# Kernel optimization log

Hardware: AMD Instinct MI355X
Metric: run time of the kernel (lower is better)

## Reference

```python
import jax, jax.numpy as jnp
import numpy as np

N_NODES = 256
BATCH = 1024
N_LAYERS = 2  # total linear layers = N_LAYERS + 1, each followed by tanh


def setup_inputs() -> dict:
    key = jax.random.key(0)
    ks = jax.random.split(key, 4)
    scale = 1.0 / np.sqrt(N_NODES)
    x = jax.random.normal(ks[0], (BATCH, N_NODES), dtype=jnp.float32)
    # nn.Linear weights: [out_features, in_features], no bias
    W0 = jax.random.normal(ks[1], (N_NODES, N_NODES), dtype=jnp.float32) * scale
    W1 = jax.random.normal(ks[2], (N_NODES, N_NODES), dtype=jnp.float32) * scale
    W2 = jax.random.normal(ks[3], (N_NODES, N_NODES), dtype=jnp.float32) * scale
    return {"x": x, "W0": W0, "W1": W1, "W2": W2}


def reference(x, W0, W1, W2):
    # Original loop: for each node i, zero out column i of x (x @ Par with
    # Par = I - e_i e_i^T), run the 3-layer tanh MLP, keep output column i.
    # Vectorized: build all N masked copies at once.
    N = x.shape[1]
    mask = (1.0 - jnp.eye(N, dtype=x.dtype))  # [i, j]: zero col j==i
    Xm = x[None, :, :] * mask[:, None, :]     # [N, B, N]
    # nn.Linear: y = h @ W.T ; tanh after every layer (incl. last)
    h = jnp.tanh(jnp.einsum('ibn,mn->ibm', Xm, W0))
    h = jnp.tanh(jnp.einsum('ibn,mn->ibm', h, W1))
    h = jnp.tanh(jnp.einsum('ibn,mn->ibm', h, W2))  # [N, B, N]
    # f_x[b, i] = h[i, b, i]
    f_x = jnp.einsum('ibi->bi', h)
    return f_x
```

## Files before the change

### kernel.cpp

```cpp
#include <hip/hip_runtime.h>
#include <hip/hip_bf16.h>

#define N_NODES 256
#define BATCH   1024

typedef __attribute__((ext_vector_type(8))) short bf16x8;
typedef __attribute__((ext_vector_type(4))) float f32x4;

__device__ __forceinline__ float ftanh(float x) {
    float e = __builtin_amdgcn_exp2f(x * 2.8853900817779268f);
    float r = __builtin_amdgcn_rcpf(e + 1.0f);
    return fmaf(-2.0f, r, 1.0f);
}

__device__ __forceinline__ unsigned short f2bf(float f) {
    unsigned u = __float_as_uint(f);
    return (unsigned short)((u + 0x7fffu + ((u >> 16) & 1u)) >> 16);
}

__device__ __forceinline__ unsigned pack_bf2(float a, float b) {
    union { __hip_bfloat162 h; unsigned u; } cvt;
    cvt.h = __float22bfloat162_rn(make_float2(a, b));
    return cvt.u;
}

template <int CTRL>
__device__ __forceinline__ float dpp_add(float s) {
    int t = __builtin_amdgcn_update_dpp(0, __float_as_int(s), CTRL, 0xf, 0xf, true);
    return s + __int_as_float(t);
}

__global__ void z0_prep(const float* __restrict__ x, const float* __restrict__ W0,
                        const float* __restrict__ W1, float* __restrict__ Z0,
                        float* __restrict__ xT, float* __restrict__ W0col,
                        unsigned short* __restrict__ W1bf) {
    __shared__ float xs[32][36];
    __shared__ float ws[32][36];
    int t = threadIdx.x;

    int gb = (blockIdx.y * 32 + blockIdx.x) * 256 + t;
    {
        int i = gb >> 8, m = gb & 255;
        W0col[gb] = W0[m * 256 + i];
        W1bf[gb]  = f2bf(W1[gb]);
    }
#pragma unroll
    for (int r = 0; r < 4; ++r) {
        int id = r * 65536 + gb;
        int i = id >> 10, b = id & 1023;
        xT[id] = x[b * 256 + i];
    }

    int b0 = blockIdx.x * 32, m0 = blockIdx.y * 32;
    int lr = t >> 3, lc = (t & 7) << 2;
    int tr = (t >> 4) << 1, tc = (t & 15) << 1;
    float acc00 = 0.f, acc01 = 0.f, acc10 = 0.f, acc11 = 0.f;
    for (int k0 = 0; k0 < 256; k0 += 32) {
        *(float4*)&xs[lr][lc] = *(const float4*)&x[(b0 + lr) * 256 + k0 + lc];
        *(float4*)&ws[lr][lc] = *(const float4*)&W0[(m0 + lr) * 256 + k0 + lc];
        __syncthreads();
#pragma unroll
        for (int k = 0; k < 32; ++k) {
            float a0 = xs[tr][k], a1 = xs[tr + 1][k];
            float w0v = ws[tc][k], w1v = ws[tc + 1][k];
            acc00 = fmaf(a0, w0v, acc00);
            acc01 = fmaf(a0, w1v, acc01);
            acc10 = fmaf(a1, w0v, acc10);
            acc11 = fmaf(a1, w1v, acc11);
        }
        __syncthreads();
    }
    Z0[(b0 + tr) * 256 + m0 + tc]         = acc00;
    Z0[(b0 + tr) * 256 + m0 + tc + 1]     = acc01;
    Z0[(b0 + tr + 1) * 256 + m0 + tc]     = acc10;
    Z0[(b0 + tr + 1) * 256 + m0 + tc + 1] = acc11;
}

__launch_bounds__(512, 4)
__global__ void fused(const float* __restrict__ Z0, const float* __restrict__ xT,
                      const float* __restrict__ W0col,
                      const unsigned short* __restrict__ W1bf,
                      const float* __restrict__ W2, float* __restrict__ out) {
    __shared__ __align__(16) unsigned char h0s[64 * 512];
    float* wavepart = (float*)h0s;
    int t  = threadIdx.x;
    int r0 = blockIdx.x * 64;
    int i  = blockIdx.y;

    int wave = t >> 6, lane = t & 63;
    int lr = lane & 15, lh = lane >> 4;

    float w2v[2];
#pragma unroll
    for (int nt = 0; nt < 2; ++nt)
        w2v[nt] = W2[i * 256 + wave * 32 + nt * 16 + lr];

    {
        int rowgrp = t >> 5, chunk = t & 31;
        int col0 = chunk << 3;
        float4 w0a = *(const float4*)&W0col[i * 256 + col0];
        float4 w0b = *(const float4*)&W0col[i * 256 + col0 + 4];
        float w[8] = {w0a.x, w0a.y, w0a.z, w0a.w, w0b.x, w0b.y, w0b.z, w0b.w};
#pragma unroll
        for (int p = 0; p < 4; ++p) {
            int row = p * 16 + rowgrp;
            float xi = xT[i * 1024 + r0 + row];
            float4 za = *(const float4*)&Z0[(r0 + row) * 256 + col0];
            float4 zb = *(const float4*)&Z0[(r0 + row) * 256 + col0 + 4];
            float z[8] = {za.x, za.y, za.z, za.w, zb.x, zb.y, zb.z, zb.w};
            unsigned pk[4];
#pragma unroll
            for (int e = 0; e < 4; ++e) {
                float ha = ftanh(fmaf(-xi, w[2 * e],     z[2 * e]));
                float hb = ftanh(fmaf(-xi, w[2 * e + 1], z[2 * e + 1]));
                pk[e] = pack_bf2(ha, hb);
            }
            uint4 v = make_uint4(pk[0], pk[1], pk[2], pk[3]);
            *(uint4*)(h0s + row * 512 + (((chunk ^ (row & 31)) << 4))) = v;
        }
    }
    __syncthreads();

    f32x4 acc[4][2];
#pragma unroll
    for (int a = 0; a < 4; ++a)
#pragma unroll
        for (int b = 0; b < 2; ++b)
            acc[a][b] = (f32x4){0.f, 0.f, 0.f, 0.f};

    const unsigned short* w1p0 = W1bf + (wave * 32 + lr) * 256 + lh * 8;
    const unsigned short* w1p1 = W1bf + (wave * 32 + 16 + lr) * 256 + lh * 8;
    bf16x8 bnext0 = *(const bf16x8*)(w1p0);
    bf16x8 bnext1 = *(const bf16x8*)(w1p1);

#pragma unroll
    for (int ks = 0; ks < 8; ++ks) {
        int kk = ks * 32 + lh * 8;
        int chunk = kk >> 3;
        bf16x8 b0 = bnext0, b1 = bnext1;
        if (ks < 7) {
            bnext0 = *(const bf16x8*)(w1p0 + (ks + 1) * 32);
            bnext1 = *(const bf16x8*)(w1p1 + (ks + 1) * 32);
        }
        bf16x8 afrag[4];
#pragma unroll
        for (int mt = 0; mt < 4; ++mt) {
            int row = mt * 16 + lr;
            afrag[mt] = *(const bf16x8*)(h0s + row * 512 + ((chunk ^ (row & 31)) << 4));
        }
#pragma unroll
        for (int mt = 0; mt < 4; ++mt) {
            acc[mt][0] = __builtin_amdgcn_mfma_f32_16x16x32_bf16(
                afrag[mt], b0, acc[mt][0], 0, 0, 0);
            acc[mt][1] = __builtin_amdgcn_mfma_f32_16x16x32_bf16(
                afrag[mt], b1, acc[mt][1], 0, 0, 0);
        }
    }

    float part[4][4];
#pragma unroll
    for (int mt = 0; mt < 4; ++mt) {
#pragma unroll
        for (int r = 0; r < 4; ++r) {
            float s = fmaf(ftanh(acc[mt][0][r]), w2v[0],
                           ftanh(acc[mt][1][r]) * w2v[1]);
            s = dpp_add<0x118>(s);
            s = dpp_add<0x114>(s);
            s = dpp_add<0x112>(s);
            s = dpp_add<0x111>(s);
            part[mt][r] = s;
        }
    }
    __syncthreads();
    if (lr == 15) {
#pragma unroll
        for (int mt = 0; mt < 4; ++mt)
#pragma unroll
            for (int r = 0; r < 4; ++r)
                wavepart[wave * 64 + mt * 16 + lh * 4 + r] = part[mt][r];
    }
    __syncthreads();

    if (t < 64) {
        float s = 0.f;
#pragma unroll
        for (int w = 0; w < 8; ++w)
            s += wavepart[w * 64 + t];
        out[(r0 + t) * 256 + i] = ftanh(s);
    }
}

extern "C" void kernel_launch(void* const* d_in, const int* in_sizes, int n_in,
                              void* d_out, int out_size, void* d_ws, size_t ws_size,
                              hipStream_t stream) {
    const float* x  = (const float*)d_in[0];
    const float* W0 = (const float*)d_in[1];
    const float* W1 = (const float*)d_in[2];
    const float* W2 = (const float*)d_in[3];
    float* out = (float*)d_out;

    char* ws = (char*)d_ws;
    float* Z0            = (float*)ws;
    float* xT            = (float*)(ws + (1 << 20));
    float* W0col         = (float*)(ws + (2 << 20));
    unsigned short* W1bf = (unsigned short*)(ws + (2 << 20) + (256 << 10));

    z0_prep<<<dim3(32, 8), 256, 0, stream>>>(x, W0, W1, Z0, xT, W0col, W1bf);
    fused<<<dim3(16, 256), 512, 0, stream>>>(Z0, xT, W0col, W1bf, W2, out);
}
```

Before: 94.68 us.

## Process four nodes per block and overlap next h0 build with MFMA

Each block of the fused kernel now handles CH=4 consecutive nodes instead of one. While the MFMA loop for the current node runs, it loads Z0, xT and W0col for the next node and computes the next tanh h0 tile into registers, so that work is software-pipelined behind the matrix ops. The final reduction for the previous node is also deferred into the next iteration. Fewer blocks are launched and occupancy is lowered to 2 blocks per CU for more registers, which reduces parallelism and adds register pressure.

```diff
diff --git a/kernel.cpp b/kernel.cpp
--- a/kernel.cpp
+++ b/kernel.cpp
@@ -3,6 +3,7 @@
 
 #define N_NODES 256
 #define BATCH   1024
+#define CH      4
 
 typedef __attribute__((ext_vector_type(8))) short bf16x8;
 typedef __attribute__((ext_vector_type(4))) float f32x4;
@@ -76,117 +77,152 @@
     Z0[(b0 + tr + 1) * 256 + m0 + tc + 1] = acc11;
 }
 
-__launch_bounds__(512, 4)
+__launch_bounds__(512, 2)
 __global__ void fused(const float* __restrict__ Z0, const float* __restrict__ xT,
                       const float* __restrict__ W0col,
                       const unsigned short* __restrict__ W1bf,
                       const float* __restrict__ W2, float* __restrict__ out) {
     __shared__ __align__(16) unsigned char h0s[64 * 512];
-    float* wavepart = (float*)h0s;
-    int t  = threadIdx.x;
-    int r0 = blockIdx.x * 64;
-    int i  = blockIdx.y;
-
-    int wave = t >> 6, lane = t & 63;
-    int lr = lane & 15, lh = lane >> 4;
-
-    float w2v[2];
-#pragma unroll
-    for (int nt = 0; nt < 2; ++nt)
-        w2v[nt] = W2[i * 256 + wave * 32 + nt * 16 + lr];
+    __shared__ float wavepart[8 * 64];
+    const int t  = threadIdx.x;
+    const int r0 = blockIdx.x * 64;
+    const int i0 = blockIdx.y * CH;
+
+    const int wave = t >> 6, lane = t & 63;
+    const int lr = lane & 15, lh = lane >> 4;
+    const int rowgrp = t >> 5, chunk = t & 31, col0 = chunk << 3;
+
+    unsigned pk[16];
 
     {
-        int rowgrp = t >> 5, chunk = t & 31;
-        int col0 = chunk << 3;
-        float4 w0a = *(const float4*)&W0col[i * 256 + col0];
-        float4 w0b = *(const float4*)&W0col[i * 256 + col0 + 4];
-        float w[8] = {w0a.x, w0a.y, w0a.z, w0a.w, w0b.x, w0b.y, w0b.z, w0b.w};
+        float4 wa = *(const float4*)&W0col[i0 * 256 + col0];
+        float4 wb = *(const float4*)&W0col[i0 * 256 + col0 + 4];
 #pragma unroll
         for (int p = 0; p < 4; ++p) {
             int row = p * 16 + rowgrp;
-            float xi = xT[i * 1024 + r0 + row];
+            float xi = xT[i0 * 1024 + r0 + row];
             float4 za = *(const float4*)&Z0[(r0 + row) * 256 + col0];
             float4 zb = *(const float4*)&Z0[(r0 + row) * 256 + col0 + 4];
-            float z[8] = {za.x, za.y, za.z, za.w, zb.x, zb.y, zb.z, zb.w};
-            unsigned pk[4];
-#pragma unroll
-            for (int e = 0; e < 4; ++e) {
-                float ha = ftanh(fmaf(-xi, w[2 * e],     z[2 * e]));
-                float hb = ftanh(fmaf(-xi, w[2 * e + 1], z[2 * e + 1]));
-                pk[e] = pack_bf2(ha, hb);
-            }
-            uint4 v = make_uint4(pk[0], pk[1], pk[2], pk[3]);
-            *(uint4*)(h0s + row * 512 + (((chunk ^ (row & 31)) << 4))) = v;
-        }
-    }
-    __syncthreads();
-
-    f32x4 acc[4][2];
-#pragma unroll
-    for (int a = 0; a < 4; ++a)
-#pragma unroll
-        for (int b = 0; b < 2; ++b)
-            acc[a][b] = (f32x4){0.f, 0.f, 0.f, 0.f};
-
-    const unsigned short* w1p0 = W1bf + (wave * 32 + lr) * 256 + lh * 8;
-    const unsigned short* w1p1 = W1bf + (wave * 32 + 16 + lr) * 256 + lh * 8;
-    bf16x8 bnext0 = *(const bf16x8*)(w1p0);
-    bf16x8 bnext1 = *(const bf16x8*)(w1p1);
-
-#pragma unroll
-    for (int ks = 0; ks < 8; ++ks) {
-        int kk = ks * 32 + lh * 8;
-        int chunk = kk >> 3;
-        bf16x8 b0 = bnext0, b1 = bnext1;
-        if (ks < 7) {
-            bnext0 = *(const bf16x8*)(w1p0 + (ks + 1) * 32);
-            bnext1 = *(const bf16x8*)(w1p1 + (ks + 1) * 32);
-        }
-        bf16x8 afrag[4];
+            pk[p * 4 + 0] = pack_bf2(ftanh(fmaf(-xi, wa.x, za.x)), ftanh(fmaf(-xi, wa.y, za.y)));
+            pk[p * 4 + 1] = pack_bf2(ftanh(fmaf(-xi, wa.z, za.z)), ftanh(fmaf(-xi, wa.w, za.w)));
+            pk[p * 4 + 2] = pack_bf2(ftanh(fmaf(-xi, wb.x, zb.x)), ftanh(fmaf(-xi, wb.y, zb.y)));
+            pk[p * 4 + 3] = pack_bf2(ftanh(fmaf(-xi, wb.z, zb.z)), ftanh(fmaf(-xi, wb.w, zb.w)));
+        }
+    }
+
+    for (int ii = 0; ii < CH; ++ii) {
+        const int i = i0 + ii;
+
+#pragma unroll
+        for (int p = 0; p < 4; ++p) {
+            int row = p * 16 + rowgrp;
+            *(uint4*)(h0s + row * 512 + ((chunk ^ (row & 31)) << 4)) =
+                make_uint4(pk[p * 4], pk[p * 4 + 1], pk[p * 4 + 2], pk[p * 4 + 3]);
+        }
+        if (ii > 0 && t < 64) {
+            float s = 0.f;
+#pragma unroll
+            for (int w = 0; w < 8; ++w) s += wavepart[w * 64 + t];
+            out[(r0 + t) * 256 + (i - 1)] = ftanh(s);
+        }
+        __syncthreads();
+
+        const float w2v0 = W2[i * 256 + wave * 32 + lr];
+        const float w2v1 = W2[i * 256 + wave * 32 + 16 + lr];
+        f32x4 acc[4][2];
+#pragma unroll
+        for (int a = 0; a < 4; ++a)
+#pragma unroll
+            for (int b = 0; b < 2; ++b)
+                acc[a][b] = (f32x4){0.f, 0.f, 0.f, 0.f};
+
+        const unsigned short* w1p0 = W1bf + (wave * 32 + lr) * 256 + lh * 8;
+        const unsigned short* w1p1 = w1p0 + 16 * 256;
+        bf16x8 bnext0 = *(const bf16x8*)(w1p0);
+        bf16x8 bnext1 = *(const bf16x8*)(w1p1);
+
+        const bool more = (ii + 1 < CH);
+        const int inx = i + 1;
+        float wn[8];
+        float4 zca, zcb, zna, znb;
+        float xic = 0.f, xin = 0.f;
+        if (more) {
+            float4 wa = *(const float4*)&W0col[inx * 256 + col0];
+            float4 wb = *(const float4*)&W0col[inx * 256 + col0 + 4];
+            wn[0]=wa.x; wn[1]=wa.y; wn[2]=wa.z; wn[3]=wa.w;
+            wn[4]=wb.x; wn[5]=wb.y; wn[6]=wb.z; wn[7]=wb.w;
+            int row = rowgrp;
+            xic = xT[inx * 1024 + r0 + row];
+            zca = *(const float4*)&Z0[(r0 + row) * 256 + col0];
+            zcb = *(const float4*)&Z0[(r0 + row) * 256 + col0 + 4];
+        }
+
+#pragma unroll
+        for (int ksv = 0; ksv < 8; ++ksv) {
+            const int p = ksv >> 1, half = ksv & 1;
+            if (half == 0 && more && p < 3) {
+                int row = (p + 1) * 16 + rowgrp;
+                xin = xT[inx * 1024 + r0 + row];
+                zna = *(const float4*)&Z0[(r0 + row) * 256 + col0];
+                znb = *(const float4*)&Z0[(r0 + row) * 256 + col0 + 4];
+            }
+            const int kk = ksv * 32 + lh * 8, ch2 = kk >> 3;
+            bf16x8 b0 = bnext0, b1 = bnext1;
+            if (ksv < 7) {
+                bnext0 = *(const bf16x8*)(w1p0 + (ksv + 1) * 32);
+                bnext1 = *(const bf16x8*)(w1p1 + (ksv + 1) * 32);
+            }
+            bf16x8 afrag[4];
+#pragma unroll
+            for (int mt = 0; mt < 4; ++mt) {
+                int row = mt * 16 + lr;
+                afrag[mt] = *(const bf16x8*)(h0s + row * 512 + ((ch2 ^ (row & 31)) << 4));
+            }
+#pragma unroll
+            for (int mt = 0; mt < 4; ++mt) {
+                acc[mt][0] = __builtin_amdgcn_mfma_f32_16x16x32_bf16(
+                    afrag[mt], b0, acc[mt][0], 0, 0, 0);
+                acc[mt][1] = __builtin_amdgcn_mfma_f32_16x16x32_bf16(
+                    afrag[mt], b1, acc[mt][1], 0, 0, 0);
+            }
+            if (more) {
+                if (half == 0) {
+                    pk[p * 4 + 0] = pack_bf2(ftanh(fmaf(-xic, wn[0], zca.x)),
+                                             ftanh(fmaf(-xic, wn[1], zca.y)));
+                    pk[p * 4 + 1] = pack_bf2(ftanh(fmaf(-xic, wn[2], zca.z)),
+                                             ftanh(fmaf(-xic, wn[3], zca.w)));
+                } else {
+                    pk[p * 4 + 2] = pack_bf2(ftanh(fmaf(-xic, wn[4], zcb.x)),
+                                             ftanh(fmaf(-xic, wn[5], zcb.y)));
+                    pk[p * 4 + 3] = pack_bf2(ftanh(fmaf(-xic, wn[6], zcb.z)),
+                                             ftanh(fmaf(-xic, wn[7], zcb.w)));
+                    if (p < 3) { xic = xin; zca = zna; zcb = znb; }
+                }
+            }
+        }
+
 #pragma unroll
         for (int mt = 0; mt < 4; ++mt) {
-            int row = mt * 16 + lr;
-            afrag[mt] = *(const bf16x8*)(h0s + row * 512 + ((chunk ^ (row & 31)) << 4));
-        }
-#pragma unroll
-        for (int mt = 0; mt < 4; ++mt) {
-            acc[mt][0] = __builtin_amdgcn_mfma_f32_16x16x32_bf16(
-                afrag[mt], b0, acc[mt][0], 0, 0, 0);
-            acc[mt][1] = __builtin_amdgcn_mfma_f32_16x16x32_bf16(
-                afrag[mt], b1, acc[mt][1], 0, 0, 0);
-        }
-    }
-
-    float part[4][4];
-#pragma unroll
-    for (int mt = 0; mt < 4; ++mt) {
-#pragma unroll
-        for (int r = 0; r < 4; ++r) {
-            float s = fmaf(ftanh(acc[mt][0][r]), w2v[0],
-                           ftanh(acc[mt][1][r]) * w2v[1]);
-            s = dpp_add<0x118>(s);
-            s = dpp_add<0x114>(s);
-            s = dpp_add<0x112>(s);
-            s = dpp_add<0x111>(s);
-            part[mt][r] = s;
-        }
-    }
-    __syncthreads();
-    if (lr == 15) {
-#pragma unroll
-        for (int mt = 0; mt < 4; ++mt)
-#pragma unroll
-            for (int r = 0; r < 4; ++r)
-                wavepart[wave * 64 + mt * 16 + lh * 4 + r] = part[mt][r];
-    }
-    __syncthreads();
+#pragma unroll
+            for (int r = 0; r < 4; ++r) {
+                float s = fmaf(ftanh(acc[mt][0][r]), w2v0,
+                               ftanh(acc[mt][1][r]) * w2v1);
+                s = dpp_add<0x118>(s);
+                s = dpp_add<0x114>(s);
+                s = dpp_add<0x112>(s);
+                s = dpp_add<0x111>(s);
+                if (lr == 15)
+                    wavepart[wave * 64 + mt * 16 + lh * 4 + r] = s;
+            }
+        }
+        __syncthreads();
+    }
 
     if (t < 64) {
         float s = 0.f;
 #pragma unroll
-        for (int w = 0; w < 8; ++w)
-            s += wavepart[w * 64 + t];
-        out[(r0 + t) * 256 + i] = ftanh(s);
+        for (int w = 0; w < 8; ++w) s += wavepart[w * 64 + t];
+        out[(r0 + t) * 256 + (i0 + CH - 1)] = ftanh(s);
     }
 }
 
@@ -206,5 +242,5 @@
     unsigned short* W1bf = (unsigned short*)(ws + (2 << 20) + (256 << 10));
 
     z0_prep<<<dim3(32, 8), 256, 0, stream>>>(x, W0, W1, Z0, xT, W0col, W1bf);
-    fused<<<dim3(16, 256), 512, 0, stream>>>(Z0, xT, W0col, W1bf, W2, out);
-}
+    fused<<<dim3(16, 256 / CH), 512, 0, stream>>>(Z0, xT, W0col, W1bf, W2, out);
+}
```

After: 105.5 us. +11.4%, slower.

## Process several masked nodes per block, keeping Z0 and W1 fragments resident

Applied to the files above, without the earlier changes.

Each fused block now handles 8 node indices instead of one. It loads its 64-row Z0 tile into shared memory once and keeps all W1 bf16 fragments in registers across those nodes. Z0 is stored as bf16 to halve its traffic, and the XOR swizzle is replaced by a padded row stride. The goal is to cut the repeated global reloads of Z0 and W1 per node. The costs are more registers (launch bounds lowered to 2 blocks), fewer blocks, extra barriers per node, and lower precision for Z0.

```diff
diff --git a/kernel.cpp b/kernel.cpp
--- a/kernel.cpp
+++ b/kernel.cpp
@@ -3,6 +3,8 @@
 
 #define N_NODES 256
 #define BATCH   1024
+#define NI      8
+#define ROWB    528
 
 typedef __attribute__((ext_vector_type(8))) short bf16x8;
 typedef __attribute__((ext_vector_type(4))) float f32x4;
@@ -24,6 +26,10 @@
     return cvt.u;
 }
 
+__device__ __forceinline__ float bf2f(short s) {
+    return __uint_as_float(((unsigned)(unsigned short)s) << 16);
+}
+
 template <int CTRL>
 __device__ __forceinline__ float dpp_add(float s) {
     int t = __builtin_amdgcn_update_dpp(0, __float_as_int(s), CTRL, 0xf, 0xf, true);
@@ -31,7 +37,8 @@
 }
 
 __global__ void z0_prep(const float* __restrict__ x, const float* __restrict__ W0,
-                        const float* __restrict__ W1, float* __restrict__ Z0,
+                        const float* __restrict__ W1,
+                        unsigned short* __restrict__ Z0bf,
                         float* __restrict__ xT, float* __restrict__ W0col,
                         unsigned short* __restrict__ W1bf) {
     __shared__ float xs[32][36];
@@ -70,123 +77,116 @@
         }
         __syncthreads();
     }
-    Z0[(b0 + tr) * 256 + m0 + tc]         = acc00;
-    Z0[(b0 + tr) * 256 + m0 + tc + 1]     = acc01;
-    Z0[(b0 + tr + 1) * 256 + m0 + tc]     = acc10;
-    Z0[(b0 + tr + 1) * 256 + m0 + tc + 1] = acc11;
-}
-
-__launch_bounds__(512, 4)
-__global__ void fused(const float* __restrict__ Z0, const float* __restrict__ xT,
+    Z0bf[(b0 + tr) * 256 + m0 + tc]         = f2bf(acc00);
+    Z0bf[(b0 + tr) * 256 + m0 + tc + 1]     = f2bf(acc01);
+    Z0bf[(b0 + tr + 1) * 256 + m0 + tc]     = f2bf(acc10);
+    Z0bf[(b0 + tr + 1) * 256 + m0 + tc + 1] = f2bf(acc11);
+}
+
+__launch_bounds__(512, 2)
+__global__ void fused(const unsigned short* __restrict__ Z0bf,
+                      const float* __restrict__ xT,
                       const float* __restrict__ W0col,
                       const unsigned short* __restrict__ W1bf,
                       const float* __restrict__ W2, float* __restrict__ out) {
-    __shared__ __align__(16) unsigned char h0s[64 * 512];
-    float* wavepart = (float*)h0s;
-    int t  = threadIdx.x;
-    int r0 = blockIdx.x * 64;
-    int i  = blockIdx.y;
-
-    int wave = t >> 6, lane = t & 63;
-    int lr = lane & 15, lh = lane >> 4;
-
-    float w2v[2];
+    __shared__ __align__(16) unsigned char z0s[64 * ROWB];
+    __shared__ __align__(16) unsigned char h0s[64 * ROWB];
+    __shared__ float wavepart[8 * 64];
+    const int t  = threadIdx.x;
+    const int r0 = blockIdx.x * 64;
+    const int i0 = blockIdx.y * NI;
+
+    const int wave = t >> 6, lane = t & 63;
+    const int lr = lane & 15, lh = lane >> 4;
+    const int rowgrp = t >> 5, chunk = t & 31, col0 = chunk << 3;
+
+#pragma unroll
+    for (int p = 0; p < 4; ++p) {
+        int row = p * 16 + rowgrp;
+        uint4 v = *(const uint4*)&Z0bf[(r0 + row) * 256 + col0];
+        *(uint4*)(z0s + row * ROWB + chunk * 16) = v;
+    }
+
+    bf16x8 w1f[2][8];
 #pragma unroll
     for (int nt = 0; nt < 2; ++nt)
-        w2v[nt] = W2[i * 256 + wave * 32 + nt * 16 + lr];
-
-    {
-        int rowgrp = t >> 5, chunk = t & 31;
-        int col0 = chunk << 3;
-        float4 w0a = *(const float4*)&W0col[i * 256 + col0];
-        float4 w0b = *(const float4*)&W0col[i * 256 + col0 + 4];
-        float w[8] = {w0a.x, w0a.y, w0a.z, w0a.w, w0b.x, w0b.y, w0b.z, w0b.w};
-#pragma unroll
-        for (int p = 0; p < 4; ++p) {
-            int row = p * 16 + rowgrp;
-            float xi = xT[i * 1024 + r0 + row];
-            float4 za = *(const float4*)&Z0[(r0 + row) * 256 + col0];
-            float4 zb = *(const float4*)&Z0[(r0 + row) * 256 + col0 + 4];
-            float z[8] = {za.x, za.y, za.z, za.w, zb.x, zb.y, zb.z, zb.w};
-            unsigned pk[4];
-#pragma unroll
-            for (int e = 0; e < 4; ++e) {
-                float ha = ftanh(fmaf(-xi, w[2 * e],     z[2 * e]));
-                float hb = ftanh(fmaf(-xi, w[2 * e + 1], z[2 * e + 1]));
-                pk[e] = pack_bf2(ha, hb);
+#pragma unroll
+        for (int ks = 0; ks < 8; ++ks)
+            w1f[nt][ks] = *(const bf16x8*)&W1bf[(wave * 32 + nt * 16 + lr) * 256 + ks * 32 + lh * 8];
+
+    __syncthreads();
+
+    for (int ii = 0; ii < NI; ++ii) {
+        const int i = i0 + ii;
+
+        {
+            float4 w0a = *(const float4*)&W0col[i * 256 + col0];
+            float4 w0b = *(const float4*)&W0col[i * 256 + col0 + 4];
+            float w[8] = {w0a.x, w0a.y, w0a.z, w0a.w, w0b.x, w0b.y, w0b.z, w0b.w};
+#pragma unroll
+            for (int p = 0; p < 4; ++p) {
+                int row = p * 16 + rowgrp;
+                float xi = xT[i * 1024 + r0 + row];
+                bf16x8 zv = *(const bf16x8*)(z0s + row * ROWB + chunk * 16);
+                unsigned pk[4];
+#pragma unroll
+                for (int e = 0; e < 4; ++e) {
+                    float ha = ftanh(fmaf(-xi, w[2 * e],     bf2f(zv[2 * e])));
+                    float hb = ftanh(fmaf(-xi, w[2 * e + 1], bf2f(zv[2 * e + 1])));
+                    pk[e] = pack_bf2(ha, hb);
+                }
+                *(uint4*)(h0s + row * ROWB + chunk * 16) =
+                    make_uint4(pk[0], pk[1], pk[2], pk[3]);
             }
-            uint4 v = make_uint4(pk[0], pk[1], pk[2], pk[3]);
-            *(uint4*)(h0s + row * 512 + (((chunk ^ (row & 31)) << 4))) = v;
-        }
-    }
-    __syncthreads();
-
-    f32x4 acc[4][2];
-#pragma unroll
-    for (int a = 0; a < 4; ++a)
-#pragma unroll
-        for (int b = 0; b < 2; ++b)
-            acc[a][b] = (f32x4){0.f, 0.f, 0.f, 0.f};
-
-    const unsigned short* w1p0 = W1bf + (wave * 32 + lr) * 256 + lh * 8;
-    const unsigned short* w1p1 = W1bf + (wave * 32 + 16 + lr) * 256 + lh * 8;
-    bf16x8 bnext0 = *(const bf16x8*)(w1p0);
-    bf16x8 bnext1 = *(const bf16x8*)(w1p1);
-
-#pragma unroll
-    for (int ks = 0; ks < 8; ++ks) {
-        int kk = ks * 32 + lh * 8;
-        int chunk = kk >> 3;
-        bf16x8 b0 = bnext0, b1 = bnext1;
-        if (ks < 7) {
-            bnext0 = *(const bf16x8*)(w1p0 + (ks + 1) * 32);
-            bnext1 = *(const bf16x8*)(w1p1 + (ks + 1) * 32);
-        }
-        bf16x8 afrag[4];
+        }
+        __syncthreads();
+
+        f32x4 acc[4][2];
+#pragma unroll
+        for (int a = 0; a < 4; ++a)
+#pragma unroll
+            for (int b = 0; b < 2; ++b)
+                acc[a][b] = (f32x4){0.f, 0.f, 0.f, 0.f};
+
+#pragma unroll
+        for (int ks = 0; ks < 8; ++ks) {
+            bf16x8 afrag[4];
+#pragma unroll
+            for (int mt = 0; mt < 4; ++mt)
+                afrag[mt] = *(const bf16x8*)(h0s + (mt * 16 + lr) * ROWB + lh * 16 + ks * 64);
+#pragma unroll
+            for (int mt = 0; mt < 4; ++mt) {
+                acc[mt][0] = __builtin_amdgcn_mfma_f32_16x16x32_bf16(
+                    afrag[mt], w1f[0][ks], acc[mt][0], 0, 0, 0);
+                acc[mt][1] = __builtin_amdgcn_mfma_f32_16x16x32_bf16(
+                    afrag[mt], w1f[1][ks], acc[mt][1], 0, 0, 0);
+            }
+        }
+
+        const float w2v0 = W2[i * 256 + wave * 32 + lr];
+        const float w2v1 = W2[i * 256 + wave * 32 + 16 + lr];
 #pragma unroll
         for (int mt = 0; mt < 4; ++mt) {
-            int row = mt * 16 + lr;
-            afrag[mt] = *(const bf16x8*)(h0s + row * 512 + ((chunk ^ (row & 31)) << 4));
-        }
-#pragma unroll
-        for (int mt = 0; mt < 4; ++mt) {
-            acc[mt][0] = __builtin_amdgcn_mfma_f32_16x16x32_bf16(
-                afrag[mt], b0, acc[mt][0], 0, 0, 0);
-            acc[mt][1] = __builtin_amdgcn_mfma_f32_16x16x32_bf16(
-                afrag[mt], b1, acc[mt][1], 0, 0, 0);
-        }
-    }
-
-    float part[4][4];
-#pragma unroll
-    for (int mt = 0; mt < 4; ++mt) {
-#pragma unroll
-        for (int r = 0; r < 4; ++r) {
-            float s = fmaf(ftanh(acc[mt][0][r]), w2v[0],
-                           ftanh(acc[mt][1][r]) * w2v[1]);
-            s = dpp_add<0x118>(s);
-            s = dpp_add<0x114>(s);
-            s = dpp_add<0x112>(s);
-            s = dpp_add<0x111>(s);
-            part[mt][r] = s;
-        }
-    }
-    __syncthreads();
-    if (lr == 15) {
-#pragma unroll
-        for (int mt = 0; mt < 4; ++mt)
-#pragma unroll
-            for (int r = 0; r < 4; ++r)
-                wavepart[wave * 64 + mt * 16 + lh * 4 + r] = part[mt][r];
-    }
-    __syncthreads();
-
-    if (t < 64) {
-        float s = 0.f;
-#pragma unroll
-        for (int w = 0; w < 8; ++w)
-            s += wavepart[w * 64 + t];
-        out[(r0 + t) * 256 + i] = ftanh(s);
+#pragma unroll
+            for (int r = 0; r < 4; ++r) {
+                float s = fmaf(ftanh(acc[mt][0][r]), w2v0,
+                               ftanh(acc[mt][1][r]) * w2v1);
+                s = dpp_add<0x118>(s);
+                s = dpp_add<0x114>(s);
+                s = dpp_add<0x112>(s);
+                s = dpp_add<0x111>(s);
+                if (lr == 15)
+                    wavepart[wave * 64 + mt * 16 + lh * 4 + r] = s;
+            }
+        }
+        __syncthreads();
+
+        if (t < 64) {
+            float s = 0.f;
+#pragma unroll
+            for (int w = 0; w < 8; ++w) s += wavepart[w * 64 + t];
+            out[(r0 + t) * 256 + i] = ftanh(s);
+        }
     }
 }
 
@@ -200,11 +200,11 @@
     float* out = (float*)d_out;
 
     char* ws = (char*)d_ws;
-    float* Z0            = (float*)ws;
-    float* xT            = (float*)(ws + (1 << 20));
-    float* W0col         = (float*)(ws + (2 << 20));
-    unsigned short* W1bf = (unsigned short*)(ws + (2 << 20) + (256 << 10));
-
-    z0_prep<<<dim3(32, 8), 256, 0, stream>>>(x, W0, W1, Z0, xT, W0col, W1bf);
-    fused<<<dim3(16, 256), 512, 0, stream>>>(Z0, xT, W0col, W1bf, W2, out);
-}
+    unsigned short* Z0bf = (unsigned short*)ws;
+    float* xT            = (float*)(ws + (512 << 10));
+    float* W0col         = (float*)(ws + (512 << 10) + (1 << 20));
+    unsigned short* W1bf = (unsigned short*)(ws + (512 << 10) + (1 << 20) + (256 << 10));
+
+    z0_prep<<<dim3(32, 8), 256, 0, stream>>>(x, W0, W1, Z0bf, xT, W0col, W1bf);
+    fused<<<dim3(16, 256 / NI), 512, 0, stream>>>(Z0bf, xT, W0col, W1bf, W2, out);
+}
```

New measurement: 89.86 us. -5.1%, faster.
